# Kernel optimization log

Measured on AMD Instinct MI355X. Metric: run time of the kernel, lower is better.

Reference implementation:

```python
import jax, jax.numpy as jnp
import numpy as np

NUM_HEADS = 16
HIDDEN = 1024
HEAD_DIM = HIDDEN // NUM_HEADS
BS, SEQ = 2, 2048


def setup_inputs() -> dict:
    key = jax.random.key(0)
    ks = jax.random.split(key, 9)
    s = 1.0 / np.sqrt(HIDDEN)
    return {
        "Q": jax.random.normal(ks[0], (BS, SEQ, HIDDEN), jnp.float32),
        "K": jax.random.normal(ks[1], (BS, SEQ, HIDDEN), jnp.float32),
        "V": jax.random.normal(ks[2], (BS, SEQ, HIDDEN), jnp.float32),
        "attention_mask": jnp.zeros((BS, 1, 1, SEQ), jnp.float32),
        # nn.Linear weights stored as [in, out] (already transposed)
        "Wq": jax.random.uniform(ks[3], (HIDDEN, HIDDEN), jnp.float32, -s, s),
        "bq": jax.random.uniform(ks[4], (HIDDEN,), jnp.float32, -s, s),
        "Wk": jax.random.uniform(ks[5], (HIDDEN, HIDDEN), jnp.float32, -s, s),
        "bk": jax.random.uniform(ks[6], (HIDDEN,), jnp.float32, -s, s),
        "Wv": jax.random.uniform(ks[7], (HIDDEN, HIDDEN), jnp.float32, -s, s),
        "bv": jax.random.uniform(ks[8], (HIDDEN,), jnp.float32, -s, s),
    }


def _split_heads(x):
    b, s, _ = x.shape
    return x.reshape(b, s, NUM_HEADS, HEAD_DIM).transpose(0, 2, 1, 3)  # [b,h,s,d]


def reference(Q, K, V, attention_mask, Wq, bq, Wk, bk, Wv, bv):
    q = _split_heads(Q @ Wq + bq)  # [b,h,s,d]
    k = _split_heads(K @ Wk + bk)
    v = _split_heads(V @ Wv + bv)
    score = jnp.einsum("bhqd,bhkd->bhqk", q, k)
    # NOTE: original adds mask BEFORE scaling by 1/sqrt(d)
    score = (score + attention_mask) / np.sqrt(HEAD_DIM)
    attn = jax.nn.softmax(score, axis=-1)
    out = jnp.einsum("bhqk,bhkd->bqhd", attn, v)  # [b,q,h,d]
    b, s = Q.shape[:2]
    return out.reshape(b, s, NUM_HEADS * HEAD_DIM)
```

## Files before the change

kernel.cpp:

```cpp
#include <hip/hip_runtime.h>
#include <hip/hip_bf16.h>
#include <stdint.h>

#define SEQ    2048
#define HIDDEN 1024
#define NH     16
#define HD     64

#define SC_LOG2E_8 0.18033688011112042f
#define SM_SHIFT   16.0f

typedef __bf16 bf16x8 __attribute__((ext_vector_type(8)));
typedef float  f32x4  __attribute__((ext_vector_type(4)));
typedef float  f32x16 __attribute__((ext_vector_type(16)));
typedef unsigned int uint32x2 __attribute__((ext_vector_type(2)));

typedef __attribute__((address_space(1))) void* as1vp;
typedef __attribute__((address_space(3))) void* as3vp;

__device__ __forceinline__ void gload_lds16(const void* g, void* l) {
  __builtin_amdgcn_global_load_lds((as1vp)(void*)g, (as3vp)l, 16, 0, 0);
}

__device__ __forceinline__ uint16_t f2bf(float f) {
  uint32_t x;
  __builtin_memcpy(&x, &f, 4);
  x += 0x7FFFu + ((x >> 16) & 1u);
  return (uint16_t)(x >> 16);
}

__device__ __forceinline__ uint32_t pkbf(float lo, float hi) {
  union { __bf16 v[2]; uint32_t u; } t;
  t.v[0] = (__bf16)lo; t.v[1] = (__bf16)hi;
  return t.u;
}

__device__ __forceinline__ uint32x2 plswap(uint32_t lo, uint32_t hi) {
  return __builtin_amdgcn_permlane32_swap(lo, hi, false, false);
}

__device__ __forceinline__ float xhalf32(float x, int lane) {
  uint32_t a;
  __builtin_memcpy(&a, &x, 4);
  uint32x2 r = plswap(a, a);
  uint32_t p = (lane < 32) ? r[1] : r[0];
  float f;
  __builtin_memcpy(&f, &p, 4);
  return f;
}

__device__ __forceinline__ float exp2_fast(float x) {
  return __builtin_amdgcn_exp2f(x);
}

__global__ __launch_bounds__(256) void k_cvt(
    const float* __restrict__ Q, const float* __restrict__ K, const float* __restrict__ V,
    const float* __restrict__ mask,
    uint16_t* __restrict__ Qb, uint16_t* __restrict__ Kb, uint16_t* __restrict__ Vb,
    float* __restrict__ mask_sc) {
  if (blockIdx.x == 2048) {
    if (blockIdx.y < 2) {
      const int i = (blockIdx.y * 256 + threadIdx.x) * 8;
      float4 a = *(const float4*)(mask + i);
      float4 b = *(const float4*)(mask + i + 4);
      a.x = a.x * SC_LOG2E_8 - SM_SHIFT; a.y = a.y * SC_LOG2E_8 - SM_SHIFT;
      a.z = a.z * SC_LOG2E_8 - SM_SHIFT; a.w = a.w * SC_LOG2E_8 - SM_SHIFT;
      b.x = b.x * SC_LOG2E_8 - SM_SHIFT; b.y = b.y * SC_LOG2E_8 - SM_SHIFT;
      b.z = b.z * SC_LOG2E_8 - SM_SHIFT; b.w = b.w * SC_LOG2E_8 - SM_SHIFT;
      *(float4*)(mask_sc + i) = a;
      *(float4*)(mask_sc + i + 4) = b;
    }
    return;
  }
  const float* src = (blockIdx.y == 0) ? Q : (blockIdx.y == 1) ? K : V;
  uint16_t*    dst = (blockIdx.y == 0) ? Qb : (blockIdx.y == 1) ? Kb : Vb;
  const int i = (blockIdx.x * 256 + threadIdx.x) * 8;
  float4 v0 = *(const float4*)(src + i);
  float4 v1 = *(const float4*)(src + i + 4);
  uint16_t tmp[8];
  tmp[0] = f2bf(v0.x); tmp[1] = f2bf(v0.y); tmp[2] = f2bf(v0.z); tmp[3] = f2bf(v0.w);
  tmp[4] = f2bf(v1.x); tmp[5] = f2bf(v1.y); tmp[6] = f2bf(v1.z); tmp[7] = f2bf(v1.w);
  __builtin_memcpy(dst + i, tmp, 16);
}

__global__ __launch_bounds__(256) void k_transpose(
    const float* __restrict__ W0, const float* __restrict__ W1, const float* __restrict__ W2,
    uint16_t* __restrict__ T0, uint16_t* __restrict__ T1, uint16_t* __restrict__ T2) {
  __shared__ uint16_t t[64][65];
  const float* W = (blockIdx.y == 0) ? W0 : (blockIdx.y == 1) ? W1 : W2;
  uint16_t*    T = (blockIdx.y == 0) ? T0 : (blockIdx.y == 1) ? T1 : T2;
  const int bx = blockIdx.x & 15, by = blockIdx.x >> 4;
  const int tx = threadIdx.x & 63, ty = threadIdx.x >> 6;
  for (int i = ty; i < 64; i += 4)
    t[i][tx] = f2bf(W[(by * 64 + i) * HIDDEN + bx * 64 + tx]);
  __syncthreads();
  for (int i = ty; i < 64; i += 4)
    T[(bx * 64 + i) * HIDDEN + by * 64 + tx] = t[tx][i];
}

__global__ __launch_bounds__(256) void k_qkv_gemm(
    const uint16_t* __restrict__ Qb, const uint16_t* __restrict__ Kb, const uint16_t* __restrict__ Vb,
    const uint16_t* __restrict__ WTq, const uint16_t* __restrict__ WTk, const uint16_t* __restrict__ WTv,
    const float* __restrict__ Bq, const float* __restrict__ Bk, const float* __restrict__ Bv,
    uint16_t* __restrict__ q_ws, uint16_t* __restrict__ k_ws, uint16_t* __restrict__ v_ws) {
  const int wg  = blockIdx.x;
  const int swz = (wg & 7) * 96 + (wg >> 3);
  const int mode = swz >> 8;
  const int rem  = swz & 255;
  const int m0   = (rem >> 3) * 128;
  const int n0   = (rem & 7) * 128;

  const uint16_t* X   = (mode == 0) ? Qb : (mode == 1) ? Kb : Vb;
  const uint16_t* WT  = (mode == 0) ? WTq : (mode == 1) ? WTk : WTv;
  const float*    bia = (mode == 0) ? Bq  : (mode == 1) ? Bk  : Bv;

  __shared__ uint16_t As[128 * 64];
  __shared__ uint16_t Bs[128 * 64];
  char* AsB = (char*)As;
  char* BsB = (char*)Bs;

  const int tid  = threadIdx.x;
  const int lane = tid & 63;
  const int w    = tid >> 6;
  const int wr   = w >> 1, wc = w & 1;

  const int lrow = lane >> 3;
  const int lcol = (lane & 7) * 16;

  f32x4 acc[4][4];
  const f32x4 zero = {0.f, 0.f, 0.f, 0.f};
#pragma unroll
  for (int i = 0; i < 4; ++i)
#pragma unroll
    for (int j = 0; j < 4; ++j) acc[i][j] = zero;

  const char* Ab = (const char*)X;
  const char* Bb = (const char*)WT;

  for (int kt = 0; kt < 16; ++kt) {
    __syncthreads();
    const int kbyte = kt * 128;
#pragma unroll
    for (int i = 0; i < 4; ++i) {
      const int r = w * 32 + i * 8;
      gload_lds16(Ab + (size_t)(m0 + r + lrow) * (HIDDEN * 2) + kbyte + lcol, AsB + r * 128);
      gload_lds16(Bb + (size_t)(n0 + r + lrow) * (HIDDEN * 2) + kbyte + lcol, BsB + r * 128);
    }
    __syncthreads();
#pragma unroll
    for (int kc = 0; kc < 2; ++kc) {
      const int chunk = kc * 64 + (lane >> 4) * 16;
      bf16x8 a[4], b[4];
#pragma unroll
      for (int f = 0; f < 4; ++f) {
        const int ra = wr * 64 + f * 16 + (lane & 15);
        a[f] = *(const bf16x8*)(AsB + ra * 128 + chunk);
        const int rb = wc * 64 + f * 16 + (lane & 15);
        b[f] = *(const bf16x8*)(BsB + rb * 128 + chunk);
      }
#pragma unroll
      for (int fm = 0; fm < 4; ++fm)
#pragma unroll
        for (int fn = 0; fn < 4; ++fn)
          acc[fm][fn] = __builtin_amdgcn_mfma_f32_16x16x32_bf16(a[fm], b[fn], acc[fm][fn], 0, 0, 0);
    }
  }

  float bfrag[4];
#pragma unroll
  for (int fn = 0; fn < 4; ++fn)
    bfrag[fn] = bia[n0 + wc * 64 + fn * 16 + (lane & 15)];

#pragma unroll
  for (int fm = 0; fm < 4; ++fm) {
    const int mrow0 = m0 + wr * 64 + fm * 16 + (lane >> 4) * 4;
    const int b0 = mrow0 >> 11;
    const int sq = mrow0 & (SEQ - 1);
#pragma unroll
    for (int fn = 0; fn < 4; ++fn) {
      const int n = n0 + wc * 64 + fn * 16 + (lane & 15);
      const int h = n >> 6, d = n & 63;
      const size_t bh = (size_t)(b0 * NH + h);
      if (mode == 2) {
        const int kt2 = sq >> 6, ks = (sq >> 4) & 3, hv = (sq >> 3) & 1, jj = sq & 7;
        const int dt = d >> 5, lnv = hv * 32 + (d & 31);
        uint16_t tmp[4];
#pragma unroll
        for (int j = 0; j < 4; ++j) tmp[j] = f2bf(acc[fm][fn][j] + bfrag[fn]);
        __builtin_memcpy(v_ws + ((((bh * 32 + kt2) * 2 + dt) * 4 + ks) * 64 + lnv) * 8 + jj,
                         tmp, 8);
      } else if (mode == 1) {
        const int kt2 = sq >> 6, c = (sq >> 5) & 1, ql = sq & 31;
        const int slot = d >> 4, hk = (d >> 3) & 1, jk = d & 7;
        uint16_t* base = k_ws + ((((bh * 32 + kt2) * 2 + c) * 4 + slot) * 64 + hk * 32 + ql) * 8 + jk;
#pragma unroll
        for (int j = 0; j < 4; ++j) base[j * 8] = f2bf(acc[fm][fn][j] + bfrag[fn]);
      } else {
        const int qt32 = sq >> 5, ql = sq & 31;
        const int slot = d >> 4, hq = (d >> 3) & 1, jq = d & 7;
        uint16_t* base = q_ws + (((bh * 64 + qt32) * 4 + slot) * 64 + hq * 32 + ql) * 8 + jq;
#pragma unroll
        for (int j = 0; j < 4; ++j)
          base[j * 8] = f2bf((acc[fm][fn][j] + bfrag[fn]) * SC_LOG2E_8);
      }
    }
  }
}

__global__ __launch_bounds__(256) void k_attn(
    const uint16_t* __restrict__ q_ws, const uint16_t* __restrict__ k_ws,
    const uint16_t* __restrict__ v_ws, const float* __restrict__ mask_sc,
    float* __restrict__ out) {
  __shared__ float smem[2][64][34];

  const int tid = threadIdx.x, lane = tid & 63, w = tid >> 6;
  const int wg  = blockIdx.x;
  const int swz = (wg & 7) * 128 + (wg >> 3);
  const int bh  = swz >> 5;
  const int qt  = swz & 31;
  const int b   = bh >> 4;
  const int h   = bh & 15;
  const int qsub = w & 1;
  const int kvh  = w >> 1;
  const int q0  = qt * 64 + qsub * 32;
  const int ql  = lane & 31;
  const int hi  = lane >> 5;

  const char* qfb = (const char*)q_ws + ((size_t)bh * 64 + (q0 >> 5)) * 4096;
  const char* kfb = (const char*)k_ws + (size_t)bh * 262144 + lane * 16;
  const char* vfb = (const char*)v_ws + (size_t)bh * 262144 + lane * 16;
  const float* mrow = mask_sc + b * SEQ;

  bf16x8 qB[4];
#pragma unroll
  for (int s = 0; s < 4; ++s)
    qB[s] = *(const bf16x8*)(qfb + s * 1024 + lane * 16);

  const f32x16 zero16 = {0.f};
  f32x16 Oacc[2];
  Oacc[0] = zero16; Oacc[1] = zero16;
  float lpart = 0.f;

  const int kbeg = kvh * 16, kend = kbeg + 16;

  for (int kt = kbeg; kt < kend; ++kt) {
    const char* kt_k = kfb + (size_t)kt * 8192;
    const char* kt_v = vfb + (size_t)kt * 8192;

    bf16x8 kf[8];
#pragma unroll
    for (int i = 0; i < 8; ++i) kf[i] = *(const bf16x8*)(kt_k + i * 1024);

    f32x16 P0, P1;
#pragma unroll
    for (int g = 0; g < 4; ++g) {
      f32x4 mk0 = *(const f32x4*)(mrow + kt * 64 + g * 8 + 4 * hi);
      f32x4 mk1 = *(const f32x4*)(mrow + kt * 64 + 32 + g * 8 + 4 * hi);
#pragma unroll
      for (int t = 0; t < 4; ++t) { P0[g * 4 + t] = mk0[t]; P1[g * 4 + t] = mk1[t]; }
    }

#pragma unroll
    for (int s = 0; s < 4; ++s)
      P0 = __builtin_amdgcn_mfma_f32_32x32x16_bf16(kf[s], qB[s], P0, 0, 0, 0);
#pragma unroll
    for (int s = 0; s < 4; ++s)
      P1 = __builtin_amdgcn_mfma_f32_32x32x16_bf16(kf[4 + s], qB[s], P1, 0, 0, 0);

    bf16x8 vA[8];
#pragma unroll
    for (int i = 0; i < 8; ++i) vA[i] = *(const bf16x8*)(kt_v + i * 1024);

    float s0 = 0.f, s1 = 0.f, s2a = 0.f, s3 = 0.f;
#pragma unroll
    for (int r = 0; r < 16; r += 4) {
      P0[r]     = exp2_fast(P0[r]);      s0  += P0[r];
      P0[r + 1] = exp2_fast(P0[r + 1]);  s1  += P0[r + 1];
      P0[r + 2] = exp2_fast(P0[r + 2]);  s2a += P0[r + 2];
      P0[r + 3] = exp2_fast(P0[r + 3]);  s3  += P0[r + 3];
      P1[r]     = exp2_fast(P1[r]);      s0  += P1[r];
      P1[r + 1] = exp2_fast(P1[r + 1]);  s1  += P1[r + 1];
      P1[r + 2] = exp2_fast(P1[r + 2]);  s2a += P1[r + 2];
      P1[r + 3] = exp2_fast(P1[r + 3]);  s3  += P1[r + 3];
    }
    lpart += (s0 + s1) + (s2a + s3);

    bf16x8 pb[4];
#pragma unroll
    for (int ks = 0; ks < 4; ++ks) {
      const int o = (ks & 1) * 8;
      uint32_t w0, w1, w2, w3;
      if (ks < 2) {
        w0 = pkbf(P0[o + 0], P0[o + 1]);
        w1 = pkbf(P0[o + 2], P0[o + 3]);
        w2 = pkbf(P0[o + 4], P0[o + 5]);
        w3 = pkbf(P0[o + 6], P0[o + 7]);
      } else {
        w0 = pkbf(P1[o + 0], P1[o + 1]);
        w1 = pkbf(P1[o + 2], P1[o + 3]);
        w2 = pkbf(P1[o + 4], P1[o + 5]);
        w3 = pkbf(P1[o + 6], P1[o + 7]);
      }
      uint32x2 r02 = plswap(w0, w2);
      uint32x2 r13 = plswap(w1, w3);
      uint32_t wv[4] = {r02[0], r13[0], r02[1], r13[1]};
      __builtin_memcpy(&pb[ks], wv, 16);
    }

#pragma unroll
    for (int ks = 0; ks < 4; ++ks) {
      Oacc[0] = __builtin_amdgcn_mfma_f32_32x32x16_bf16(vA[ks],     pb[ks], Oacc[0], 0, 0, 0);
      Oacc[1] = __builtin_amdgcn_mfma_f32_32x32x16_bf16(vA[4 + ks], pb[ks], Oacc[1], 0, 0, 0);
    }
  }

  if (kvh == 1) {
    float* s = smem[qsub][lane];
#pragma unroll
    for (int r = 0; r < 16; ++r) { s[r] = Oacc[0][r]; s[16 + r] = Oacc[1][r]; }
    s[32] = lpart;
  }
  __syncthreads();
  if (kvh == 1) return;

  const float* s = smem[qsub][lane];
  const float lt = lpart + s[32];
  const float ltot = lt + xhalf32(lt, lane);
  const float linv = 1.f / ltot;
  float* orow = out + ((size_t)(b * SEQ) + q0 + ql) * HIDDEN + h * HD;
#pragma unroll
  for (int dt = 0; dt < 2; ++dt)
#pragma unroll
    for (int g = 0; g < 4; ++g) {
      f32x4 o;
#pragma unroll
      for (int t = 0; t < 4; ++t) {
        const int r = g * 4 + t;
        o[t] = (Oacc[dt][r] + s[dt * 16 + r]) * linv;
      }
      *(f32x4*)(orow + dt * 32 + g * 8 + 4 * hi) = o;
    }
}

extern "C" void kernel_launch(void* const* d_in, const int* in_sizes, int n_in,
                              void* d_out, int out_size, void* d_ws, size_t ws_size,
                              hipStream_t stream) {
  (void)in_sizes; (void)n_in; (void)out_size; (void)ws_size;
  const float* Q    = (const float*)d_in[0];
  const float* K    = (const float*)d_in[1];
  const float* V    = (const float*)d_in[2];
  const float* mask = (const float*)d_in[3];
  const float* Wq   = (const float*)d_in[4];
  const float* bq   = (const float*)d_in[5];
  const float* Wk   = (const float*)d_in[6];
  const float* bk   = (const float*)d_in[7];
  const float* Wv   = (const float*)d_in[8];
  const float* bv   = (const float*)d_in[9];

  uint16_t* ws   = (uint16_t*)d_ws;
  uint16_t* wt_q = ws;
  uint16_t* wt_k = wt_q + HIDDEN * HIDDEN;
  uint16_t* wt_v = wt_k + HIDDEN * HIDDEN;
  const size_t qkv = (size_t)2 * SEQ * HIDDEN;
  uint16_t* Qb   = wt_v + HIDDEN * HIDDEN;
  uint16_t* Kb   = Qb + qkv;
  uint16_t* Vb   = Kb + qkv;
  uint16_t* q_ws = Vb + qkv;
  uint16_t* k_ws = q_ws + qkv;
  uint16_t* v_ws = k_ws + qkv;
  float* mask_sc = (float*)(v_ws + qkv);

  k_cvt<<<dim3(2049, 3), 256, 0, stream>>>(Q, K, V, mask, Qb, Kb, Vb, mask_sc);
  k_transpose<<<dim3(256, 3), 256, 0, stream>>>(Wq, Wk, Wv, wt_q, wt_k, wt_v);
  k_qkv_gemm<<<dim3(768), 256, 0, stream>>>(
      Qb, Kb, Vb, wt_q, wt_k, wt_v, bq, bk, bv, q_ws, k_ws, v_ws);
  k_attn<<<dim3(1024), 256, 0, stream>>>(q_ws, k_ws, v_ws, mask_sc,
                                         (float*)d_out);
}
```

Baseline: 131.9 us.

## Fuse fp32-to-bf16 input conversion into QKV GEMM and split attention KV four ways

The separate pass that converts Q/K/V to bf16 is removed. The GEMM now loads fp32 activations straight into LDS, doubling that tile to 32KB, and packs them to bf16 when reading fragments. This saves a full write and re-read of the bf16 copies, at the cost of more LDS traffic and conversion work inside the GEMM loop. Separately, the attention kernel now gives each block 32 queries with four waves each covering a quarter of the KV range, reduced through LDS, and launches twice as many blocks.

```diff
diff --git a/kernel.cpp b/kernel.cpp
--- a/kernel.cpp
+++ b/kernel.cpp
@@ -53,34 +53,17 @@
   return __builtin_amdgcn_exp2f(x);
 }
 
-__global__ __launch_bounds__(256) void k_cvt(
-    const float* __restrict__ Q, const float* __restrict__ K, const float* __restrict__ V,
-    const float* __restrict__ mask,
-    uint16_t* __restrict__ Qb, uint16_t* __restrict__ Kb, uint16_t* __restrict__ Vb,
-    float* __restrict__ mask_sc) {
-  if (blockIdx.x == 2048) {
-    if (blockIdx.y < 2) {
-      const int i = (blockIdx.y * 256 + threadIdx.x) * 8;
-      float4 a = *(const float4*)(mask + i);
-      float4 b = *(const float4*)(mask + i + 4);
-      a.x = a.x * SC_LOG2E_8 - SM_SHIFT; a.y = a.y * SC_LOG2E_8 - SM_SHIFT;
-      a.z = a.z * SC_LOG2E_8 - SM_SHIFT; a.w = a.w * SC_LOG2E_8 - SM_SHIFT;
-      b.x = b.x * SC_LOG2E_8 - SM_SHIFT; b.y = b.y * SC_LOG2E_8 - SM_SHIFT;
-      b.z = b.z * SC_LOG2E_8 - SM_SHIFT; b.w = b.w * SC_LOG2E_8 - SM_SHIFT;
-      *(float4*)(mask_sc + i) = a;
-      *(float4*)(mask_sc + i + 4) = b;
-    }
-    return;
-  }
-  const float* src = (blockIdx.y == 0) ? Q : (blockIdx.y == 1) ? K : V;
-  uint16_t*    dst = (blockIdx.y == 0) ? Qb : (blockIdx.y == 1) ? Kb : Vb;
+__global__ __launch_bounds__(256) void k_mask(
+    const float* __restrict__ mask, float* __restrict__ mask_sc) {
   const int i = (blockIdx.x * 256 + threadIdx.x) * 8;
-  float4 v0 = *(const float4*)(src + i);
-  float4 v1 = *(const float4*)(src + i + 4);
-  uint16_t tmp[8];
-  tmp[0] = f2bf(v0.x); tmp[1] = f2bf(v0.y); tmp[2] = f2bf(v0.z); tmp[3] = f2bf(v0.w);
-  tmp[4] = f2bf(v1.x); tmp[5] = f2bf(v1.y); tmp[6] = f2bf(v1.z); tmp[7] = f2bf(v1.w);
-  __builtin_memcpy(dst + i, tmp, 16);
+  float4 a = *(const float4*)(mask + i);
+  float4 b = *(const float4*)(mask + i + 4);
+  a.x = a.x * SC_LOG2E_8 - SM_SHIFT; a.y = a.y * SC_LOG2E_8 - SM_SHIFT;
+  a.z = a.z * SC_LOG2E_8 - SM_SHIFT; a.w = a.w * SC_LOG2E_8 - SM_SHIFT;
+  b.x = b.x * SC_LOG2E_8 - SM_SHIFT; b.y = b.y * SC_LOG2E_8 - SM_SHIFT;
+  b.z = b.z * SC_LOG2E_8 - SM_SHIFT; b.w = b.w * SC_LOG2E_8 - SM_SHIFT;
+  *(float4*)(mask_sc + i) = a;
+  *(float4*)(mask_sc + i + 4) = b;
 }
 
 __global__ __launch_bounds__(256) void k_transpose(
@@ -99,7 +82,7 @@
 }
 
 __global__ __launch_bounds__(256) void k_qkv_gemm(
-    const uint16_t* __restrict__ Qb, const uint16_t* __restrict__ Kb, const uint16_t* __restrict__ Vb,
+    const float* __restrict__ Qf, const float* __restrict__ Kf, const float* __restrict__ Vf,
     const uint16_t* __restrict__ WTq, const uint16_t* __restrict__ WTk, const uint16_t* __restrict__ WTv,
     const float* __restrict__ Bq, const float* __restrict__ Bk, const float* __restrict__ Bv,
     uint16_t* __restrict__ q_ws, uint16_t* __restrict__ k_ws, uint16_t* __restrict__ v_ws) {
@@ -110,11 +93,11 @@
   const int m0   = (rem >> 3) * 128;
   const int n0   = (rem & 7) * 128;
 
-  const uint16_t* X   = (mode == 0) ? Qb : (mode == 1) ? Kb : Vb;
+  const float*    X   = (mode == 0) ? Qf : (mode == 1) ? Kf : Vf;
   const uint16_t* WT  = (mode == 0) ? WTq : (mode == 1) ? WTk : WTv;
   const float*    bia = (mode == 0) ? Bq  : (mode == 1) ? Bk  : Bv;
 
-  __shared__ uint16_t As[128 * 64];
+  __shared__ float    As[128 * 64];
   __shared__ uint16_t Bs[128 * 64];
   char* AsB = (char*)As;
   char* BsB = (char*)Bs;
@@ -124,9 +107,6 @@
   const int w    = tid >> 6;
   const int wr   = w >> 1, wc = w & 1;
 
-  const int lrow = lane >> 3;
-  const int lcol = (lane & 7) * 16;
-
   f32x4 acc[4][4];
   const f32x4 zero = {0.f, 0.f, 0.f, 0.f};
 #pragma unroll
@@ -139,24 +119,33 @@
 
   for (int kt = 0; kt < 16; ++kt) {
     __syncthreads();
-    const int kbyte = kt * 128;
+#pragma unroll
+    for (int i = 0; i < 8; ++i) {
+      const int r = w * 32 + i * 4;
+      gload_lds16(Ab + (size_t)(m0 + r + (lane >> 4)) * 4096 + kt * 256 + (lane & 15) * 16,
+                  AsB + r * 256);
+    }
 #pragma unroll
     for (int i = 0; i < 4; ++i) {
       const int r = w * 32 + i * 8;
-      gload_lds16(Ab + (size_t)(m0 + r + lrow) * (HIDDEN * 2) + kbyte + lcol, AsB + r * 128);
-      gload_lds16(Bb + (size_t)(n0 + r + lrow) * (HIDDEN * 2) + kbyte + lcol, BsB + r * 128);
+      gload_lds16(Bb + (size_t)(n0 + r + (lane >> 3)) * 2048 + kt * 128 + (lane & 7) * 16,
+                  BsB + r * 128);
     }
     __syncthreads();
 #pragma unroll
     for (int kc = 0; kc < 2; ++kc) {
-      const int chunk = kc * 64 + (lane >> 4) * 16;
       bf16x8 a[4], b[4];
 #pragma unroll
       for (int f = 0; f < 4; ++f) {
         const int ra = wr * 64 + f * 16 + (lane & 15);
-        a[f] = *(const bf16x8*)(AsB + ra * 128 + chunk);
+        const char* ap = AsB + ra * 256 + kc * 128 + (lane >> 4) * 32;
+        f32x4 lo = *(const f32x4*)ap;
+        f32x4 hi = *(const f32x4*)(ap + 16);
+        uint32_t uv[4] = {pkbf(lo[0], lo[1]), pkbf(lo[2], lo[3]),
+                          pkbf(hi[0], hi[1]), pkbf(hi[2], hi[3])};
+        __builtin_memcpy(&a[f], uv, 16);
         const int rb = wc * 64 + f * 16 + (lane & 15);
-        b[f] = *(const bf16x8*)(BsB + rb * 128 + chunk);
+        b[f] = *(const bf16x8*)(BsB + rb * 128 + kc * 64 + (lane >> 4) * 16);
       }
 #pragma unroll
       for (int fm = 0; fm < 4; ++fm)
@@ -211,22 +200,20 @@
     const uint16_t* __restrict__ q_ws, const uint16_t* __restrict__ k_ws,
     const uint16_t* __restrict__ v_ws, const float* __restrict__ mask_sc,
     float* __restrict__ out) {
-  __shared__ float smem[2][64][34];
+  __shared__ float smem[3][64][33];
 
   const int tid = threadIdx.x, lane = tid & 63, w = tid >> 6;
   const int wg  = blockIdx.x;
-  const int swz = (wg & 7) * 128 + (wg >> 3);
-  const int bh  = swz >> 5;
-  const int qt  = swz & 31;
+  const int swz = (wg & 7) * 256 + (wg >> 3);
+  const int bh  = swz >> 6;
+  const int qt  = swz & 63;
   const int b   = bh >> 4;
   const int h   = bh & 15;
-  const int qsub = w & 1;
-  const int kvh  = w >> 1;
-  const int q0  = qt * 64 + qsub * 32;
+  const int q0  = qt * 32;
   const int ql  = lane & 31;
   const int hi  = lane >> 5;
 
-  const char* qfb = (const char*)q_ws + ((size_t)bh * 64 + (q0 >> 5)) * 4096;
+  const char* qfb = (const char*)q_ws + ((size_t)bh * 64 + qt) * 4096;
   const char* kfb = (const char*)k_ws + (size_t)bh * 262144 + lane * 16;
   const char* vfb = (const char*)v_ws + (size_t)bh * 262144 + lane * 16;
   const float* mrow = mask_sc + b * SEQ;
@@ -241,7 +228,7 @@
   Oacc[0] = zero16; Oacc[1] = zero16;
   float lpart = 0.f;
 
-  const int kbeg = kvh * 16, kend = kbeg + 16;
+  const int kbeg = w * 8, kend = kbeg + 8;
 
   for (int kt = kbeg; kt < kend; ++kt) {
     const char* kt_k = kfb + (size_t)kt * 8192;
@@ -314,18 +301,24 @@
     }
   }
 
-  if (kvh == 1) {
-    float* s = smem[qsub][lane];
+  if (w > 0) {
+    float* s = smem[w - 1][lane];
 #pragma unroll
     for (int r = 0; r < 16; ++r) { s[r] = Oacc[0][r]; s[16 + r] = Oacc[1][r]; }
     s[32] = lpart;
   }
   __syncthreads();
-  if (kvh == 1) return;
-
-  const float* s = smem[qsub][lane];
-  const float lt = lpart + s[32];
-  const float ltot = lt + xhalf32(lt, lane);
+  if (w > 0) return;
+
+#pragma unroll
+  for (int p = 0; p < 3; ++p) {
+    const float* s = smem[p][lane];
+#pragma unroll
+    for (int r = 0; r < 16; ++r) { Oacc[0][r] += s[r]; Oacc[1][r] += s[16 + r]; }
+    lpart += s[32];
+  }
+
+  const float ltot = lpart + xhalf32(lpart, lane);
   const float linv = 1.f / ltot;
   float* orow = out + ((size_t)(b * SEQ) + q0 + ql) * HIDDEN + h * HD;
 #pragma unroll
@@ -334,10 +327,7 @@
     for (int g = 0; g < 4; ++g) {
       f32x4 o;
 #pragma unroll
-      for (int t = 0; t < 4; ++t) {
-        const int r = g * 4 + t;
-        o[t] = (Oacc[dt][r] + s[dt * 16 + r]) * linv;
-      }
+      for (int t = 0; t < 4; ++t) o[t] = Oacc[dt][g * 4 + t] * linv;
       *(f32x4*)(orow + dt * 32 + g * 8 + 4 * hi) = o;
     }
 }
@@ -362,18 +352,15 @@
   uint16_t* wt_k = wt_q + HIDDEN * HIDDEN;
   uint16_t* wt_v = wt_k + HIDDEN * HIDDEN;
   const size_t qkv = (size_t)2 * SEQ * HIDDEN;
-  uint16_t* Qb   = wt_v + HIDDEN * HIDDEN;
-  uint16_t* Kb   = Qb + qkv;
-  uint16_t* Vb   = Kb + qkv;
-  uint16_t* q_ws = Vb + qkv;
+  uint16_t* q_ws = wt_v + HIDDEN * HIDDEN;
   uint16_t* k_ws = q_ws + qkv;
   uint16_t* v_ws = k_ws + qkv;
   float* mask_sc = (float*)(v_ws + qkv);
 
-  k_cvt<<<dim3(2049, 3), 256, 0, stream>>>(Q, K, V, mask, Qb, Kb, Vb, mask_sc);
+  k_mask<<<dim3(2), 256, 0, stream>>>(mask, mask_sc);
   k_transpose<<<dim3(256, 3), 256, 0, stream>>>(Wq, Wk, Wv, wt_q, wt_k, wt_v);
   k_qkv_gemm<<<dim3(768), 256, 0, stream>>>(
-      Qb, Kb, Vb, wt_q, wt_k, wt_v, bq, bk, bv, q_ws, k_ws, v_ws);
-  k_attn<<<dim3(1024), 256, 0, stream>>>(q_ws, k_ws, v_ws, mask_sc,
+      Q, K, V, wt_q, wt_k, wt_v, bq, bk, bv, q_ws, k_ws, v_ws);
+  k_attn<<<dim3(2048), 256, 0, stream>>>(q_ws, k_ws, v_ws, mask_sc,
                                          (float*)d_out);
 }
```

Result: slower. 160.5 us (+21.8%).

## Process two 32-row query tiles per wave to reuse K/V fragments

Applied to the files above, without the earlier changes.

Each wave now handles 64 query rows (two 32-row sub-tiles) instead of 32, so every K and V fragment loaded from global memory feeds twice as many MFMAs. The grid is halved to 512 workgroups, the swizzle and shared-memory reduction buffer are resized, and launch_bounds is dropped. This cuts K/V load traffic per FLOP, at the cost of many more live registers (four score and four output accumulators) and fewer workgroups to spread across the GPU.

```diff
diff --git a/kernel.cpp b/kernel.cpp
--- a/kernel.cpp
+++ b/kernel.cpp
@@ -207,39 +207,40 @@
   }
 }
 
-__global__ __launch_bounds__(256) void k_attn(
+__global__ void k_attn(
     const uint16_t* __restrict__ q_ws, const uint16_t* __restrict__ k_ws,
     const uint16_t* __restrict__ v_ws, const float* __restrict__ mask_sc,
     float* __restrict__ out) {
-  __shared__ float smem[2][64][34];
+  __shared__ float smem[2][64][66];
 
   const int tid = threadIdx.x, lane = tid & 63, w = tid >> 6;
   const int wg  = blockIdx.x;
-  const int swz = (wg & 7) * 128 + (wg >> 3);
-  const int bh  = swz >> 5;
-  const int qt  = swz & 31;
+  const int swz = (wg & 7) * 64 + (wg >> 3);
+  const int bh  = swz >> 4;
+  const int qt  = swz & 15;
   const int b   = bh >> 4;
   const int h   = bh & 15;
-  const int qsub = w & 1;
-  const int kvh  = w >> 1;
-  const int q0  = qt * 64 + qsub * 32;
+  const int p   = w & 1;
+  const int kvh = w >> 1;
+  const int q0  = qt * 128 + p * 64;
   const int ql  = lane & 31;
   const int hi  = lane >> 5;
 
-  const char* qfb = (const char*)q_ws + ((size_t)bh * 64 + (q0 >> 5)) * 4096;
+  const char* qfa = (const char*)q_ws + ((size_t)bh * 64 + (q0 >> 5)) * 4096;
   const char* kfb = (const char*)k_ws + (size_t)bh * 262144 + lane * 16;
   const char* vfb = (const char*)v_ws + (size_t)bh * 262144 + lane * 16;
   const float* mrow = mask_sc + b * SEQ;
 
-  bf16x8 qB[4];
-#pragma unroll
-  for (int s = 0; s < 4; ++s)
-    qB[s] = *(const bf16x8*)(qfb + s * 1024 + lane * 16);
+  bf16x8 qBa[4], qBb[4];
+#pragma unroll
+  for (int s = 0; s < 4; ++s) {
+    qBa[s] = *(const bf16x8*)(qfa + s * 1024 + lane * 16);
+    qBb[s] = *(const bf16x8*)(qfa + 4096 + s * 1024 + lane * 16);
+  }
 
   const f32x16 zero16 = {0.f};
-  f32x16 Oacc[2];
-  Oacc[0] = zero16; Oacc[1] = zero16;
-  float lpart = 0.f;
+  f32x16 Oa0 = zero16, Oa1 = zero16, Ob0 = zero16, Ob1 = zero16;
+  float la = 0.f, lb = 0.f;
 
   const int kbeg = kvh * 16, kend = kbeg + 16;
 
@@ -247,99 +248,162 @@
     const char* kt_k = kfb + (size_t)kt * 8192;
     const char* kt_v = vfb + (size_t)kt * 8192;
 
-    bf16x8 kf[8];
-#pragma unroll
-    for (int i = 0; i < 8; ++i) kf[i] = *(const bf16x8*)(kt_k + i * 1024);
-
-    f32x16 P0, P1;
+    f32x16 Pa0, Pa1, Pb0, Pb1;
 #pragma unroll
     for (int g = 0; g < 4; ++g) {
       f32x4 mk0 = *(const f32x4*)(mrow + kt * 64 + g * 8 + 4 * hi);
       f32x4 mk1 = *(const f32x4*)(mrow + kt * 64 + 32 + g * 8 + 4 * hi);
 #pragma unroll
-      for (int t = 0; t < 4; ++t) { P0[g * 4 + t] = mk0[t]; P1[g * 4 + t] = mk1[t]; }
-    }
-
-#pragma unroll
-    for (int s = 0; s < 4; ++s)
-      P0 = __builtin_amdgcn_mfma_f32_32x32x16_bf16(kf[s], qB[s], P0, 0, 0, 0);
-#pragma unroll
-    for (int s = 0; s < 4; ++s)
-      P1 = __builtin_amdgcn_mfma_f32_32x32x16_bf16(kf[4 + s], qB[s], P1, 0, 0, 0);
+      for (int t = 0; t < 4; ++t) {
+        Pa0[g * 4 + t] = mk0[t]; Pa1[g * 4 + t] = mk1[t];
+        Pb0[g * 4 + t] = mk0[t]; Pb1[g * 4 + t] = mk1[t];
+      }
+    }
+
+    {
+      bf16x8 kf[4];
+#pragma unroll
+      for (int i = 0; i < 4; ++i) kf[i] = *(const bf16x8*)(kt_k + i * 1024);
+#pragma unroll
+      for (int s = 0; s < 4; ++s)
+        Pa0 = __builtin_amdgcn_mfma_f32_32x32x16_bf16(kf[s], qBa[s], Pa0, 0, 0, 0);
+#pragma unroll
+      for (int s = 0; s < 4; ++s)
+        Pb0 = __builtin_amdgcn_mfma_f32_32x32x16_bf16(kf[s], qBb[s], Pb0, 0, 0, 0);
+#pragma unroll
+      for (int i = 0; i < 4; ++i) kf[i] = *(const bf16x8*)(kt_k + 4096 + i * 1024);
+#pragma unroll
+      for (int s = 0; s < 4; ++s)
+        Pa1 = __builtin_amdgcn_mfma_f32_32x32x16_bf16(kf[s], qBa[s], Pa1, 0, 0, 0);
+#pragma unroll
+      for (int s = 0; s < 4; ++s)
+        Pb1 = __builtin_amdgcn_mfma_f32_32x32x16_bf16(kf[s], qBb[s], Pb1, 0, 0, 0);
+    }
+
+    bf16x8 pba[4], pbb[4];
+    {
+      float s0 = 0.f, s1 = 0.f, s2 = 0.f, s3 = 0.f;
+#pragma unroll
+      for (int r = 0; r < 16; r += 4) {
+        Pa0[r]     = exp2_fast(Pa0[r]);      s0 += Pa0[r];
+        Pa0[r + 1] = exp2_fast(Pa0[r + 1]);  s1 += Pa0[r + 1];
+        Pa0[r + 2] = exp2_fast(Pa0[r + 2]);  s2 += Pa0[r + 2];
+        Pa0[r + 3] = exp2_fast(Pa0[r + 3]);  s3 += Pa0[r + 3];
+        Pa1[r]     = exp2_fast(Pa1[r]);      s0 += Pa1[r];
+        Pa1[r + 1] = exp2_fast(Pa1[r + 1]);  s1 += Pa1[r + 1];
+        Pa1[r + 2] = exp2_fast(Pa1[r + 2]);  s2 += Pa1[r + 2];
+        Pa1[r + 3] = exp2_fast(Pa1[r + 3]);  s3 += Pa1[r + 3];
+      }
+      la += (s0 + s1) + (s2 + s3);
+#pragma unroll
+      for (int ks = 0; ks < 4; ++ks) {
+        const int o = (ks & 1) * 8;
+        uint32_t w0, w1, w2, w3;
+        if (ks < 2) {
+          w0 = pkbf(Pa0[o + 0], Pa0[o + 1]); w1 = pkbf(Pa0[o + 2], Pa0[o + 3]);
+          w2 = pkbf(Pa0[o + 4], Pa0[o + 5]); w3 = pkbf(Pa0[o + 6], Pa0[o + 7]);
+        } else {
+          w0 = pkbf(Pa1[o + 0], Pa1[o + 1]); w1 = pkbf(Pa1[o + 2], Pa1[o + 3]);
+          w2 = pkbf(Pa1[o + 4], Pa1[o + 5]); w3 = pkbf(Pa1[o + 6], Pa1[o + 7]);
+        }
+        uint32x2 r02 = plswap(w0, w2);
+        uint32x2 r13 = plswap(w1, w3);
+        uint32_t wv[4] = {r02[0], r13[0], r02[1], r13[1]};
+        __builtin_memcpy(&pba[ks], wv, 16);
+      }
+    }
 
     bf16x8 vA[8];
 #pragma unroll
     for (int i = 0; i < 8; ++i) vA[i] = *(const bf16x8*)(kt_v + i * 1024);
 
-    float s0 = 0.f, s1 = 0.f, s2a = 0.f, s3 = 0.f;
-#pragma unroll
-    for (int r = 0; r < 16; r += 4) {
-      P0[r]     = exp2_fast(P0[r]);      s0  += P0[r];
-      P0[r + 1] = exp2_fast(P0[r + 1]);  s1  += P0[r + 1];
-      P0[r + 2] = exp2_fast(P0[r + 2]);  s2a += P0[r + 2];
-      P0[r + 3] = exp2_fast(P0[r + 3]);  s3  += P0[r + 3];
-      P1[r]     = exp2_fast(P1[r]);      s0  += P1[r];
-      P1[r + 1] = exp2_fast(P1[r + 1]);  s1  += P1[r + 1];
-      P1[r + 2] = exp2_fast(P1[r + 2]);  s2a += P1[r + 2];
-      P1[r + 3] = exp2_fast(P1[r + 3]);  s3  += P1[r + 3];
-    }
-    lpart += (s0 + s1) + (s2a + s3);
-
-    bf16x8 pb[4];
+    {
+      float s0 = 0.f, s1 = 0.f, s2 = 0.f, s3 = 0.f;
+#pragma unroll
+      for (int r = 0; r < 16; r += 4) {
+        Pb0[r]     = exp2_fast(Pb0[r]);      s0 += Pb0[r];
+        Pb0[r + 1] = exp2_fast(Pb0[r + 1]);  s1 += Pb0[r + 1];
+        Pb0[r + 2] = exp2_fast(Pb0[r + 2]);  s2 += Pb0[r + 2];
+        Pb0[r + 3] = exp2_fast(Pb0[r + 3]);  s3 += Pb0[r + 3];
+        Pb1[r]     = exp2_fast(Pb1[r]);      s0 += Pb1[r];
+        Pb1[r + 1] = exp2_fast(Pb1[r + 1]);  s1 += Pb1[r + 1];
+        Pb1[r + 2] = exp2_fast(Pb1[r + 2]);  s2 += Pb1[r + 2];
+        Pb1[r + 3] = exp2_fast(Pb1[r + 3]);  s3 += Pb1[r + 3];
+      }
+      lb += (s0 + s1) + (s2 + s3);
+#pragma unroll
+      for (int ks = 0; ks < 4; ++ks) {
+        const int o = (ks & 1) * 8;
+        uint32_t w0, w1, w2, w3;
+        if (ks < 2) {
+          w0 = pkbf(Pb0[o + 0], Pb0[o + 1]); w1 = pkbf(Pb0[o + 2], Pb0[o + 3]);
+          w2 = pkbf(Pb0[o + 4], Pb0[o + 5]); w3 = pkbf(Pb0[o + 6], Pb0[o + 7]);
+        } else {
+          w0 = pkbf(Pb1[o + 0], Pb1[o + 1]); w1 = pkbf(Pb1[o + 2], Pb1[o + 3]);
+          w2 = pkbf(Pb1[o + 4], Pb1[o + 5]); w3 = pkbf(Pb1[o + 6], Pb1[o + 7]);
+        }
+        uint32x2 r02 = plswap(w0, w2);
+        uint32x2 r13 = plswap(w1, w3);
+        uint32_t wv[4] = {r02[0], r13[0], r02[1], r13[1]};
+        __builtin_memcpy(&pbb[ks], wv, 16);
+      }
+    }
+
 #pragma unroll
     for (int ks = 0; ks < 4; ++ks) {
-      const int o = (ks & 1) * 8;
-      uint32_t w0, w1, w2, w3;
-      if (ks < 2) {
-        w0 = pkbf(P0[o + 0], P0[o + 1]);
-        w1 = pkbf(P0[o + 2], P0[o + 3]);
-        w2 = pkbf(P0[o + 4], P0[o + 5]);
-        w3 = pkbf(P0[o + 6], P0[o + 7]);
-      } else {
-        w0 = pkbf(P1[o + 0], P1[o + 1]);
-        w1 = pkbf(P1[o + 2], P1[o + 3]);
-        w2 = pkbf(P1[o + 4], P1[o + 5]);
-        w3 = pkbf(P1[o + 6], P1[o + 7]);
-      }
-      uint32x2 r02 = plswap(w0, w2);
-      uint32x2 r13 = plswap(w1, w3);
-      uint32_t wv[4] = {r02[0], r13[0], r02[1], r13[1]};
-      __builtin_memcpy(&pb[ks], wv, 16);
-    }
-
+      Oa0 = __builtin_amdgcn_mfma_f32_32x32x16_bf16(vA[ks],     pba[ks], Oa0, 0, 0, 0);
+      Oa1 = __builtin_amdgcn_mfma_f32_32x32x16_bf16(vA[4 + ks], pba[ks], Oa1, 0, 0, 0);
+    }
 #pragma unroll
     for (int ks = 0; ks < 4; ++ks) {
-      Oacc[0] = __builtin_amdgcn_mfma_f32_32x32x16_bf16(vA[ks],     pb[ks], Oacc[0], 0, 0, 0);
-      Oacc[1] = __builtin_amdgcn_mfma_f32_32x32x16_bf16(vA[4 + ks], pb[ks], Oacc[1], 0, 0, 0);
+      Ob0 = __builtin_amdgcn_mfma_f32_32x32x16_bf16(vA[ks],     pbb[ks], Ob0, 0, 0, 0);
+      Ob1 = __builtin_amdgcn_mfma_f32_32x32x16_bf16(vA[4 + ks], pbb[ks], Ob1, 0, 0, 0);
     }
   }
 
   if (kvh == 1) {
-    float* s = smem[qsub][lane];
-#pragma unroll
-    for (int r = 0; r < 16; ++r) { s[r] = Oacc[0][r]; s[16 + r] = Oacc[1][r]; }
-    s[32] = lpart;
+    float* s = smem[p][lane];
+#pragma unroll
+    for (int r = 0; r < 16; ++r) {
+      s[r] = Oa0[r]; s[16 + r] = Oa1[r];
+      s[33 + r] = Ob0[r]; s[49 + r] = Ob1[r];
+    }
+    s[32] = la; s[65] = lb;
   }
   __syncthreads();
   if (kvh == 1) return;
 
-  const float* s = smem[qsub][lane];
-  const float lt = lpart + s[32];
-  const float ltot = lt + xhalf32(lt, lane);
-  const float linv = 1.f / ltot;
-  float* orow = out + ((size_t)(b * SEQ) + q0 + ql) * HIDDEN + h * HD;
-#pragma unroll
-  for (int dt = 0; dt < 2; ++dt)
-#pragma unroll
-    for (int g = 0; g < 4; ++g) {
-      f32x4 o;
-#pragma unroll
-      for (int t = 0; t < 4; ++t) {
-        const int r = g * 4 + t;
-        o[t] = (Oacc[dt][r] + s[dt * 16 + r]) * linv;
-      }
-      *(f32x4*)(orow + dt * 32 + g * 8 + 4 * hi) = o;
-    }
+  const float* s = smem[p][lane];
+#pragma unroll
+  for (int r = 0; r < 16; ++r) {
+    Oa0[r] += s[r]; Oa1[r] += s[16 + r];
+    Ob0[r] += s[33 + r]; Ob1[r] += s[49 + r];
+  }
+  la += s[32]; lb += s[65];
+
+  const float lat = la + xhalf32(la, lane);
+  const float lbt = lb + xhalf32(lb, lane);
+  const float lia = 1.f / lat;
+  const float lib = 1.f / lbt;
+
+  float* orowa = out + ((size_t)(b * SEQ) + q0 + ql) * HIDDEN + h * HD;
+  float* orowb = out + ((size_t)(b * SEQ) + q0 + 32 + ql) * HIDDEN + h * HD;
+#pragma unroll
+  for (int g = 0; g < 4; ++g) {
+    f32x4 o;
+#pragma unroll
+    for (int t = 0; t < 4; ++t) o[t] = Oa0[g * 4 + t] * lia;
+    *(f32x4*)(orowa + g * 8 + 4 * hi) = o;
+#pragma unroll
+    for (int t = 0; t < 4; ++t) o[t] = Oa1[g * 4 + t] * lia;
+    *(f32x4*)(orowa + 32 + g * 8 + 4 * hi) = o;
+#pragma unroll
+    for (int t = 0; t < 4; ++t) o[t] = Ob0[g * 4 + t] * lib;
+    *(f32x4*)(orowb + g * 8 + 4 * hi) = o;
+#pragma unroll
+    for (int t = 0; t < 4; ++t) o[t] = Ob1[g * 4 + t] * lib;
+    *(f32x4*)(orowb + 32 + g * 8 + 4 * hi) = o;
+  }
 }
 
 extern "C" void kernel_launch(void* const* d_in, const int* in_sizes, int n_in,
@@ -374,6 +438,6 @@
   k_transpose<<<dim3(256, 3), 256, 0, stream>>>(Wq, Wk, Wv, wt_q, wt_k, wt_v);
   k_qkv_gemm<<<dim3(768), 256, 0, stream>>>(
       Qb, Kb, Vb, wt_q, wt_k, wt_v, bq, bk, bv, q_ws, k_ws, v_ws);
-  k_attn<<<dim3(1024), 256, 0, stream>>>(q_ws, k_ws, v_ws, mask_sc,
-                                         (float*)d_out);
-}
+  k_attn<<<dim3(512), 256, 0, stream>>>(q_ws, k_ws, v_ws, mask_sc,
+                                        (float*)d_out);
+}
```

Measured after the change: 436.8 us. 3.31x slower.
